# Kernel optimization log

Measured on AMD Instinct MI355X. Metric: run time of the kernel, lower is better.

The kernel has to match this reference:

```python
import jax, jax.numpy as jnp
import numpy as np

N = 50000
E = 800000
F_IN = 128
F_HID = 256   # 2 * out_channels
F_OUT = 128


def setup_inputs() -> dict:
    key = jax.random.key(0)
    ks = jax.random.split(key, 6)
    x = jax.random.normal(ks[0], (N, F_IN), dtype=jnp.float32)
    edge_index = jax.random.randint(ks[1], (2, E), 0, N, dtype=jnp.int64)
    # GCNConv params: glorot weight + zero bias (PyG default)
    s1 = (6.0 / (F_IN + F_HID)) ** 0.5
    s2 = (6.0 / (F_HID + F_OUT)) ** 0.5
    W1 = jax.random.uniform(ks[2], (F_IN, F_HID), jnp.float32, -s1, s1)
    b1 = jnp.zeros((F_HID,), jnp.float32)
    W2 = jax.random.uniform(ks[3], (F_HID, F_OUT), jnp.float32, -s2, s2)
    b2 = jnp.zeros((F_OUT,), jnp.float32)
    return {"x": x, "edge_index": edge_index, "W1": W1, "b1": b1, "W2": W2, "b2": b2}


def _gcn_conv(x, W, b, src, dst, deg_inv_sqrt, n):
    # norm per edge (self-loops already appended to src/dst)
    norm = deg_inv_sqrt[src] * deg_inv_sqrt[dst]          # [E+N]
    h = x @ W                                             # [N, F_out]
    msg = h[src] * norm[:, None]                          # [E+N, F_out] gather
    out = jax.ops.segment_sum(msg, dst, num_segments=n)   # scatter-add
    return out + b


def reference(x, edge_index, W1, b1, W2, b2):
    n = x.shape[0]
    loops = jnp.arange(n, dtype=edge_index.dtype)
    src = jnp.concatenate([edge_index[0], loops])
    dst = jnp.concatenate([edge_index[1], loops])
    # symmetric normalization with self-loops (PyG GCNConv default)
    deg = jax.ops.segment_sum(jnp.ones_like(dst, dtype=x.dtype), dst, num_segments=n)
    deg_inv_sqrt = jnp.where(deg > 0, jax.lax.rsqrt(jnp.maximum(deg, 1e-12)), 0.0)
    h = jax.nn.relu(_gcn_conv(x, W1, b1, src, dst, deg_inv_sqrt, n))
    h = jax.nn.relu(_gcn_conv(h, W2, b2, src, dst, deg_inv_sqrt, n))
    return h
```

## Files before the change

kernel.cpp:

```cpp
#include <hip/hip_runtime.h>


typedef short bf16x8 __attribute__((ext_vector_type(8)));
typedef float f32x4 __attribute__((ext_vector_type(4)));

#define LDSTRIDE 264
#define BSHIFT 7
#define BMASK 127

__device__ inline unsigned short f2bf(float f) {
    unsigned int u = __float_as_uint(f);
    u += 0x7FFF + ((u >> 16) & 1);
    return (unsigned short)(u >> 16);
}
__device__ inline float bf2f(unsigned short h) {
    return __uint_as_float(((unsigned int)h) << 16);
}

__device__ inline void swz1(const float* W, unsigned short* Ws, int K, int N, int i) {
    int k = i / N, n = i % N;
    int KC = K >> 5;
    size_t d = ((((size_t)(n >> 4) * KC + (k >> 5)) * 64) + ((k >> 3) & 3) * 16 + (n & 15)) * 8
               + (k & 7);
    Ws[d] = f2bf(W[i]);
}
__global__ void wswz_kernel(const float* __restrict__ W1, const float* __restrict__ W2,
                            unsigned short* __restrict__ W1s, unsigned short* __restrict__ W2s,
                            int* __restrict__ ctrl) {
    int i = blockIdx.x * blockDim.x + threadIdx.x;
    if (blockIdx.x == 0) {
        for (int j = threadIdx.x; j < 512; j += 256) ctrl[j] = 0;
    }
    if (i < 32768) swz1(W1, W1s, 128, 256, i);
    else if (i < 65536) swz1(W2, W2s, 256, 128, i - 32768);
}

__global__ __launch_bounds__(256) void bin_kernel(
    const int* __restrict__ src, const int* __restrict__ dst,
    int* __restrict__ bcur, unsigned int* __restrict__ bbuf,
    int E, int cap, int nbuck) {
    __shared__ int cnt[512];
    __shared__ int base[512];
    int t = threadIdx.x;
    for (int i = t; i < nbuck; i += 256) cnt[i] = 0;
    __syncthreads();
    int e0 = blockIdx.x * 2048;
    unsigned int p_[8];
    int b_[8];
#pragma unroll
    for (int i = 0; i < 8; i++) {
        int e = e0 + i * 256 + t;
        if (e < E) {
            int s = src[e], d = dst[e];
            b_[i] = d >> BSHIFT;
            p_[i] = ((unsigned)(d & BMASK) << 24) | (unsigned)s;
            atomicAdd(&cnt[b_[i]], 1);
        } else b_[i] = -1;
    }
    __syncthreads();
    for (int b = t; b < nbuck; b += 256) {
        int c = cnt[b];
        base[b] = (c > 0) ? atomicAdd(&bcur[b], c) : 0;
    }
    __syncthreads();
    for (int i = t; i < nbuck; i += 256) cnt[i] = 0;
    __syncthreads();
#pragma unroll
    for (int i = 0; i < 8; i++) {
        if (b_[i] >= 0) {
            int b = b_[i];
            int p = base[b] + atomicAdd(&cnt[b], 1);
            if (p >= 0 && p < cap) bbuf[(size_t)b * cap + p] = p_[i];
        }
    }
}

__global__ __launch_bounds__(256) void bucket_csr_kernel(
    const int* __restrict__ bcur, const unsigned int* __restrict__ bbuf,
    const float* __restrict__ x,
    int* __restrict__ col, int* __restrict__ rowbeg, int* __restrict__ rowend,
    float* __restrict__ dinv, unsigned short* __restrict__ Xs, int N, int cap) {
    __shared__ int ldeg[128];
    __shared__ int lrp[256];
    __shared__ float sdv[128];
    int b = blockIdx.x, t = threadIdx.x;
    int cnt = min(max(bcur[b], 0), cap);
    if (t < 128) ldeg[t] = 0;
    __syncthreads();
    const unsigned int* mybuf = bbuf + (size_t)b * cap;
    for (int i = t; i < cnt; i += 256)
        atomicAdd(&ldeg[mybuf[i] >> 24], 1);
    __syncthreads();
    int v = (t < 128) ? ldeg[t] : 0;
    lrp[t] = v;
    __syncthreads();
    for (int off = 1; off < 128; off <<= 1) {
        int u = (t >= off) ? lrp[t - off] : 0;
        __syncthreads();
        lrp[t] += u;
        __syncthreads();
    }
    int excl = lrp[t] - v;
    int gbase = b * cap;
    if (t < 128) {
        int r = b * 128 + t;
        float dv = rsqrtf((float)v + 1.0f);
        sdv[t] = dv;
        if (r < N) {
            rowbeg[r] = gbase + excl;
            rowend[r] = gbase + excl + v;
            dinv[r] = dv;
        }
        ldeg[t] = excl;
    }
    __syncthreads();
    for (int i = t; i < cnt; i += 256) {
        unsigned int pr = mybuf[i];
        int p = atomicAdd(&ldeg[pr >> 24], 1);
        col[gbase + p] = (int)(pr & 0xffffffu);
    }
    int rbase = b * 128;
    for (int i = t; i < 128 * 32; i += 256) {
        int rl = i >> 5;
        int gr = rbase + rl;
        if (gr >= N) break;
        float s = sdv[rl];
        float4 xv = ((const float4*)x)[(size_t)gr * 32 + (i & 31)];
        ushort4 o;
        o.x = f2bf(xv.x * s); o.y = f2bf(xv.y * s);
        o.z = f2bf(xv.z * s); o.w = f2bf(xv.w * s);
        ((ushort4*)Xs)[(size_t)gr * 32 + (i & 31)] = o;
    }
}

__global__ __launch_bounds__(256) void gather2_kernel(
    const int* __restrict__ rowbeg, const int* __restrict__ rowend,
    const int* __restrict__ col, const unsigned short* __restrict__ P,
    const float* __restrict__ dinv, const float* __restrict__ bias,
    float* __restrict__ OF, int N) {
    int gid = blockIdx.x * blockDim.x + threadIdx.x;
    int r = gid >> 5;
    if (r >= N) return;
    int lane = gid & 31;
    const size_t off = (size_t)lane * 4;
    const unsigned short* Pf = P + off;

    ushort4 u = *(const ushort4*)(Pf + (size_t)r * 128);
    float ax = bf2f(u.x), ay = bf2f(u.y), az = bf2f(u.z), aw = bf2f(u.w);

    int beg = rowbeg[r], end = rowend[r];
    int i = beg;
    for (; i + 7 < end; i += 8) {
        ushort4 v0 = *(const ushort4*)(Pf + (size_t)col[i + 0] * 128);
        ushort4 v1 = *(const ushort4*)(Pf + (size_t)col[i + 1] * 128);
        ushort4 v2 = *(const ushort4*)(Pf + (size_t)col[i + 2] * 128);
        ushort4 v3 = *(const ushort4*)(Pf + (size_t)col[i + 3] * 128);
        ushort4 v4 = *(const ushort4*)(Pf + (size_t)col[i + 4] * 128);
        ushort4 v5 = *(const ushort4*)(Pf + (size_t)col[i + 5] * 128);
        ushort4 v6 = *(const ushort4*)(Pf + (size_t)col[i + 6] * 128);
        ushort4 v7 = *(const ushort4*)(Pf + (size_t)col[i + 7] * 128);
        ax += bf2f(v0.x) + bf2f(v1.x) + bf2f(v2.x) + bf2f(v3.x)
            + bf2f(v4.x) + bf2f(v5.x) + bf2f(v6.x) + bf2f(v7.x);
        ay += bf2f(v0.y) + bf2f(v1.y) + bf2f(v2.y) + bf2f(v3.y)
            + bf2f(v4.y) + bf2f(v5.y) + bf2f(v6.y) + bf2f(v7.y);
        az += bf2f(v0.z) + bf2f(v1.z) + bf2f(v2.z) + bf2f(v3.z)
            + bf2f(v4.z) + bf2f(v5.z) + bf2f(v6.z) + bf2f(v7.z);
        aw += bf2f(v0.w) + bf2f(v1.w) + bf2f(v2.w) + bf2f(v3.w)
            + bf2f(v4.w) + bf2f(v5.w) + bf2f(v6.w) + bf2f(v7.w);
    }
    for (; i < end; i++) {
        ushort4 a = *(const ushort4*)(Pf + (size_t)col[i] * 128);
        ax += bf2f(a.x); ay += bf2f(a.y); az += bf2f(a.z); aw += bf2f(a.w);
    }
    float s = dinv[r];
    float4 bb = *(const float4*)(bias + off);
    float4 o;
    o.x = fmaxf(ax * s + bb.x, 0.f);
    o.y = fmaxf(ay * s + bb.y, 0.f);
    o.z = fmaxf(az * s + bb.z, 0.f);
    o.w = fmaxf(aw * s + bb.w, 0.f);
    *(float4*)(OF + (size_t)r * 128 + off) = o;
}

__global__ __launch_bounds__(256, 4) void gemm_fused_kernel(
    const int* __restrict__ rowbeg, const int* __restrict__ rowend,
    const int* __restrict__ col, const unsigned short* __restrict__ Xs,
    const unsigned short* __restrict__ W1s, const unsigned short* __restrict__ W2s,
    const float* __restrict__ bias, const float* __restrict__ dinv,
    unsigned short* __restrict__ T, int M) {
    __shared__ unsigned short lh[4][16 * LDSTRIDE];
    int wave = threadIdx.x >> 6;
    int lane = threadIdx.x & 63;
    int mt = blockIdx.x * 4 + wave;
    int m0 = mt * 16;
    bool active = (m0 < M);
    int mrow = lane & 15, quad = lane >> 4;
    unsigned short* myl = lh[wave];

    if (active) {
        int rr = m0 + mrow; if (rr >= M) rr = M - 1;
        float acc[4][8];
        const unsigned short* base = Xs + quad * 8;
#pragma unroll
        for (int kc = 0; kc < 4; kc++) {
            bf16x8 v = *(const bf16x8*)(base + (size_t)rr * 128 + kc * 32);
#pragma unroll
            for (int j = 0; j < 8; j++) acc[kc][j] = bf2f((unsigned short)v[j]);
        }
        int beg = rowbeg[rr], end = rowend[rr];
        int i = beg;
        for (; i + 3 < end; i += 4) {
            size_t c0 = (size_t)col[i] * 128, c1 = (size_t)col[i + 1] * 128;
            size_t c2 = (size_t)col[i + 2] * 128, c3 = (size_t)col[i + 3] * 128;
            bf16x8 p0 = *(const bf16x8*)(base + c0);
            bf16x8 p1 = *(const bf16x8*)(base + c0 + 32);
            bf16x8 p2 = *(const bf16x8*)(base + c0 + 64);
            bf16x8 p3 = *(const bf16x8*)(base + c0 + 96);
            bf16x8 q0 = *(const bf16x8*)(base + c1);
            bf16x8 q1 = *(const bf16x8*)(base + c1 + 32);
            bf16x8 q2 = *(const bf16x8*)(base + c1 + 64);
            bf16x8 q3 = *(const bf16x8*)(base + c1 + 96);
            bf16x8 r0 = *(const bf16x8*)(base + c2);
            bf16x8 r1 = *(const bf16x8*)(base + c2 + 32);
            bf16x8 r2 = *(const bf16x8*)(base + c2 + 64);
            bf16x8 r3 = *(const bf16x8*)(base + c2 + 96);
            bf16x8 s0 = *(const bf16x8*)(base + c3);
            bf16x8 s1 = *(const bf16x8*)(base + c3 + 32);
            bf16x8 s2 = *(const bf16x8*)(base + c3 + 64);
            bf16x8 s3 = *(const bf16x8*)(base + c3 + 96);
#pragma unroll
            for (int j = 0; j < 8; j++) {
                acc[0][j] += (bf2f((unsigned short)p0[j]) + bf2f((unsigned short)q0[j]))
                           + (bf2f((unsigned short)r0[j]) + bf2f((unsigned short)s0[j]));
                acc[1][j] += (bf2f((unsigned short)p1[j]) + bf2f((unsigned short)q1[j]))
                           + (bf2f((unsigned short)r1[j]) + bf2f((unsigned short)s1[j]));
                acc[2][j] += (bf2f((unsigned short)p2[j]) + bf2f((unsigned short)q2[j]))
                           + (bf2f((unsigned short)r2[j]) + bf2f((unsigned short)s2[j]));
                acc[3][j] += (bf2f((unsigned short)p3[j]) + bf2f((unsigned short)q3[j]))
                           + (bf2f((unsigned short)r3[j]) + bf2f((unsigned short)s3[j]));
            }
        }
        for (; i + 1 < end; i += 2) {
            size_t c0 = (size_t)col[i] * 128, c1 = (size_t)col[i + 1] * 128;
            bf16x8 p0 = *(const bf16x8*)(base + c0);
            bf16x8 p1 = *(const bf16x8*)(base + c0 + 32);
            bf16x8 p2 = *(const bf16x8*)(base + c0 + 64);
            bf16x8 p3 = *(const bf16x8*)(base + c0 + 96);
            bf16x8 q0 = *(const bf16x8*)(base + c1);
            bf16x8 q1 = *(const bf16x8*)(base + c1 + 32);
            bf16x8 q2 = *(const bf16x8*)(base + c1 + 64);
            bf16x8 q3 = *(const bf16x8*)(base + c1 + 96);
#pragma unroll
            for (int j = 0; j < 8; j++) {
                acc[0][j] += bf2f((unsigned short)p0[j]) + bf2f((unsigned short)q0[j]);
                acc[1][j] += bf2f((unsigned short)p1[j]) + bf2f((unsigned short)q1[j]);
                acc[2][j] += bf2f((unsigned short)p2[j]) + bf2f((unsigned short)q2[j]);
                acc[3][j] += bf2f((unsigned short)p3[j]) + bf2f((unsigned short)q3[j]);
            }
        }
        if (i < end) {
            size_t c0 = (size_t)col[i] * 128;
#pragma unroll
            for (int kc = 0; kc < 4; kc++) {
                bf16x8 p = *(const bf16x8*)(base + c0 + kc * 32);
#pragma unroll
                for (int j = 0; j < 8; j++) acc[kc][j] += bf2f((unsigned short)p[j]);
            }
        }
        float dvr = dinv[rr];
        bf16x8 a[4];
#pragma unroll
        for (int kc = 0; kc < 4; kc++)
#pragma unroll
            for (int j = 0; j < 8; j++)
                a[kc][j] = (short)f2bf(acc[kc][j] * dvr);

        float dv[4];
#pragma unroll
        for (int i2 = 0; i2 < 4; i2++) {
            int gr = m0 + quad * 4 + i2;
            dv[i2] = dinv[gr < M ? gr : M - 1];
        }
        const bf16x8* w1v = (const bf16x8*)W1s;
        for (int nt = 0; nt < 16; nt++) {
            f32x4 c = {0.f, 0.f, 0.f, 0.f};
#pragma unroll
            for (int kc = 0; kc < 4; kc++) {
                bf16x8 b = w1v[(nt * 4 + kc) * 64 + lane];
                c = __builtin_amdgcn_mfma_f32_16x16x32_bf16(a[kc], b, c, 0, 0, 0);
            }
            int colc = nt * 16 + mrow;
            float bb = bias[colc];
#pragma unroll
            for (int i2 = 0; i2 < 4; i2++) {
                float v = fmaxf(c[i2] + bb, 0.f) * dv[i2];
                myl[(quad * 4 + i2) * LDSTRIDE + colc] = f2bf(v);
            }
        }
    }
    __syncthreads();
    if (active) {
        bf16x8 h[8];
        const unsigned short* hrow = myl + mrow * LDSTRIDE + quad * 8;
#pragma unroll
        for (int kc = 0; kc < 8; kc++) h[kc] = *(const bf16x8*)(hrow + kc * 32);
        const bf16x8* w2v = (const bf16x8*)W2s;
        for (int nt = 0; nt < 8; nt++) {
            f32x4 c = {0.f, 0.f, 0.f, 0.f};
#pragma unroll
            for (int kc = 0; kc < 8; kc++) {
                bf16x8 b = w2v[(nt * 8 + kc) * 64 + lane];
                c = __builtin_amdgcn_mfma_f32_16x16x32_bf16(h[kc], b, c, 0, 0, 0);
            }
            int colc = nt * 16 + mrow;
#pragma unroll
            for (int i2 = 0; i2 < 4; i2++) {
                int gr = m0 + quad * 4 + i2;
                if (gr < M) T[(size_t)gr * 128 + colc] = f2bf(c[i2]);
            }
        }
    }
}

extern "C" void kernel_launch(void* const* d_in, const int* in_sizes, int n_in,
                              void* d_out, int out_size, void* d_ws, size_t ws_size,
                              hipStream_t stream) {
    const float* x  = (const float*)d_in[0];
    const int* ei   = (const int*)d_in[1];
    const float* W1 = (const float*)d_in[2];
    const float* b1 = (const float*)d_in[3];
    const float* W2 = (const float*)d_in[4];
    const float* b2 = (const float*)d_in[5];
    float* out      = (float*)d_out;

    const int N = in_sizes[0] / 128;
    const int E = in_sizes[1] / 2;
    const int* src = ei;
    const int* dst = ei + E;

    const int nbuck = (N + BMASK) >> BSHIFT;
    const int cap = E / nbuck + E / (4 * nbuck) + 512;

    float* ws = (float*)d_ws;
    size_t Np = ((size_t)N + 255) & ~(size_t)255;
    float*          dinv = ws;
    unsigned short* Ts   = (unsigned short*)(dinv + Np);
    unsigned short* Xs   = Ts + (size_t)N * 128;
    unsigned short* W1s  = Xs + (size_t)N * 128;
    unsigned short* W2s  = W1s + 32768;
    int* rowbeg = (int*)(W2s + 32768);
    int* rowend = rowbeg + Np;
    int* ctrl   = rowend + Np;
    int* bcur   = ctrl;
    unsigned int* bbuf = (unsigned int*)(ctrl + 512);
    int* col    = (int*)(bbuf + (size_t)nbuck * cap);

    wswz_kernel<<<256, 256, 0, stream>>>(W1, W2, W1s, W2s, ctrl);
    int nbins = (E + 2047) / 2048;
    bin_kernel<<<nbins, 256, 0, stream>>>(src, dst, bcur, bbuf, E, cap, nbuck);
    bucket_csr_kernel<<<nbuck, 256, 0, stream>>>(bcur, bbuf, x, col, rowbeg, rowend,
                                                 dinv, Xs, N, cap);

    int mtiles = (N + 15) / 16;
    gemm_fused_kernel<<<(mtiles + 3) / 4, 256, 0, stream>>>(rowbeg, rowend, col, Xs,
                                                            W1s, W2s, b1, dinv, Ts, N);

    int gth = N * 32;
    gather2_kernel<<<(gth + 255) / 256, 256, 0, stream>>>(rowbeg, rowend, col, Ts,
                                                          dinv, b2, out, N);
}
```

Baseline: 209.7 us.

## Split each 16-row tile across two waves for gather and both GEMMs

The fused aggregate+GEMM kernel now assigns one 16-row tile to a 128-thread block of two waves instead of four independent tiles per 256-thread block. Each wave gathers half of every row's neighbor list, and the partial sums are combined through LDS. The two waves then split the output columns of both MFMA GEMMs. The intent is to double parallelism per tile and shorten the latency-bound gather chain, at the cost of extra LDS traffic, three block barriers and more launched blocks.

```diff
diff --git a/kernel.cpp b/kernel.cpp
--- a/kernel.cpp
+++ b/kernel.cpp
@@ -182,142 +182,176 @@
     *(float4*)(OF + (size_t)r * 128 + off) = o;
 }
 
-__global__ __launch_bounds__(256, 4) void gemm_fused_kernel(
+__global__ __launch_bounds__(128, 6) void gemm_fused_kernel(
     const int* __restrict__ rowbeg, const int* __restrict__ rowend,
     const int* __restrict__ col, const unsigned short* __restrict__ Xs,
     const unsigned short* __restrict__ W1s, const unsigned short* __restrict__ W2s,
     const float* __restrict__ bias, const float* __restrict__ dinv,
     unsigned short* __restrict__ T, int M) {
-    __shared__ unsigned short lh[4][16 * LDSTRIDE];
+    __shared__ unsigned short afr[16 * 136];
+    __shared__ float part[16 * 132];
+    unsigned short* Hl = (unsigned short*)part;
+
     int wave = threadIdx.x >> 6;
     int lane = threadIdx.x & 63;
-    int mt = blockIdx.x * 4 + wave;
-    int m0 = mt * 16;
-    bool active = (m0 < M);
+    int m0 = blockIdx.x * 16;
     int mrow = lane & 15, quad = lane >> 4;
-    unsigned short* myl = lh[wave];
-
-    if (active) {
-        int rr = m0 + mrow; if (rr >= M) rr = M - 1;
-        float acc[4][8];
-        const unsigned short* base = Xs + quad * 8;
+
+    int rr = m0 + mrow; if (rr >= M) rr = M - 1;
+    float acc[4][8];
+    const unsigned short* base = Xs + quad * 8;
+    int beg = rowbeg[rr], end = rowend[rr];
+    int half = (end - beg) >> 1;
+    int b0 = wave ? (beg + half) : beg;
+    int e0 = wave ? end : (beg + half);
+
+    if (wave == 0) {
 #pragma unroll
         for (int kc = 0; kc < 4; kc++) {
             bf16x8 v = *(const bf16x8*)(base + (size_t)rr * 128 + kc * 32);
 #pragma unroll
             for (int j = 0; j < 8; j++) acc[kc][j] = bf2f((unsigned short)v[j]);
         }
-        int beg = rowbeg[rr], end = rowend[rr];
-        int i = beg;
-        for (; i + 3 < end; i += 4) {
-            size_t c0 = (size_t)col[i] * 128, c1 = (size_t)col[i + 1] * 128;
-            size_t c2 = (size_t)col[i + 2] * 128, c3 = (size_t)col[i + 3] * 128;
-            bf16x8 p0 = *(const bf16x8*)(base + c0);
-            bf16x8 p1 = *(const bf16x8*)(base + c0 + 32);
-            bf16x8 p2 = *(const bf16x8*)(base + c0 + 64);
-            bf16x8 p3 = *(const bf16x8*)(base + c0 + 96);
-            bf16x8 q0 = *(const bf16x8*)(base + c1);
-            bf16x8 q1 = *(const bf16x8*)(base + c1 + 32);
-            bf16x8 q2 = *(const bf16x8*)(base + c1 + 64);
-            bf16x8 q3 = *(const bf16x8*)(base + c1 + 96);
-            bf16x8 r0 = *(const bf16x8*)(base + c2);
-            bf16x8 r1 = *(const bf16x8*)(base + c2 + 32);
-            bf16x8 r2 = *(const bf16x8*)(base + c2 + 64);
-            bf16x8 r3 = *(const bf16x8*)(base + c2 + 96);
-            bf16x8 s0 = *(const bf16x8*)(base + c3);
-            bf16x8 s1 = *(const bf16x8*)(base + c3 + 32);
-            bf16x8 s2 = *(const bf16x8*)(base + c3 + 64);
-            bf16x8 s3 = *(const bf16x8*)(base + c3 + 96);
-#pragma unroll
-            for (int j = 0; j < 8; j++) {
-                acc[0][j] += (bf2f((unsigned short)p0[j]) + bf2f((unsigned short)q0[j]))
-                           + (bf2f((unsigned short)r0[j]) + bf2f((unsigned short)s0[j]));
-                acc[1][j] += (bf2f((unsigned short)p1[j]) + bf2f((unsigned short)q1[j]))
-                           + (bf2f((unsigned short)r1[j]) + bf2f((unsigned short)s1[j]));
-                acc[2][j] += (bf2f((unsigned short)p2[j]) + bf2f((unsigned short)q2[j]))
-                           + (bf2f((unsigned short)r2[j]) + bf2f((unsigned short)s2[j]));
-                acc[3][j] += (bf2f((unsigned short)p3[j]) + bf2f((unsigned short)q3[j]))
-                           + (bf2f((unsigned short)r3[j]) + bf2f((unsigned short)s3[j]));
+    } else {
+#pragma unroll
+        for (int kc = 0; kc < 4; kc++)
+#pragma unroll
+            for (int j = 0; j < 8; j++) acc[kc][j] = 0.f;
+    }
+
+    int i = b0;
+    for (; i + 3 < e0; i += 4) {
+        size_t c0 = (size_t)col[i] * 128, c1 = (size_t)col[i + 1] * 128;
+        size_t c2 = (size_t)col[i + 2] * 128, c3 = (size_t)col[i + 3] * 128;
+        bf16x8 p0 = *(const bf16x8*)(base + c0);
+        bf16x8 p1 = *(const bf16x8*)(base + c0 + 32);
+        bf16x8 p2 = *(const bf16x8*)(base + c0 + 64);
+        bf16x8 p3 = *(const bf16x8*)(base + c0 + 96);
+        bf16x8 q0 = *(const bf16x8*)(base + c1);
+        bf16x8 q1 = *(const bf16x8*)(base + c1 + 32);
+        bf16x8 q2 = *(const bf16x8*)(base + c1 + 64);
+        bf16x8 q3 = *(const bf16x8*)(base + c1 + 96);
+        bf16x8 r0 = *(const bf16x8*)(base + c2);
+        bf16x8 r1 = *(const bf16x8*)(base + c2 + 32);
+        bf16x8 r2 = *(const bf16x8*)(base + c2 + 64);
+        bf16x8 r3 = *(const bf16x8*)(base + c2 + 96);
+        bf16x8 s0 = *(const bf16x8*)(base + c3);
+        bf16x8 s1 = *(const bf16x8*)(base + c3 + 32);
+        bf16x8 s2 = *(const bf16x8*)(base + c3 + 64);
+        bf16x8 s3 = *(const bf16x8*)(base + c3 + 96);
+#pragma unroll
+        for (int j = 0; j < 8; j++) {
+            acc[0][j] += (bf2f((unsigned short)p0[j]) + bf2f((unsigned short)q0[j]))
+                       + (bf2f((unsigned short)r0[j]) + bf2f((unsigned short)s0[j]));
+            acc[1][j] += (bf2f((unsigned short)p1[j]) + bf2f((unsigned short)q1[j]))
+                       + (bf2f((unsigned short)r1[j]) + bf2f((unsigned short)s1[j]));
+            acc[2][j] += (bf2f((unsigned short)p2[j]) + bf2f((unsigned short)q2[j]))
+                       + (bf2f((unsigned short)r2[j]) + bf2f((unsigned short)s2[j]));
+            acc[3][j] += (bf2f((unsigned short)p3[j]) + bf2f((unsigned short)q3[j]))
+                       + (bf2f((unsigned short)r3[j]) + bf2f((unsigned short)s3[j]));
+        }
+    }
+    for (; i + 1 < e0; i += 2) {
+        size_t c0 = (size_t)col[i] * 128, c1 = (size_t)col[i + 1] * 128;
+        bf16x8 p0 = *(const bf16x8*)(base + c0);
+        bf16x8 p1 = *(const bf16x8*)(base + c0 + 32);
+        bf16x8 p2 = *(const bf16x8*)(base + c0 + 64);
+        bf16x8 p3 = *(const bf16x8*)(base + c0 + 96);
+        bf16x8 q0 = *(const bf16x8*)(base + c1);
+        bf16x8 q1 = *(const bf16x8*)(base + c1 + 32);
+        bf16x8 q2 = *(const bf16x8*)(base + c1 + 64);
+        bf16x8 q3 = *(const bf16x8*)(base + c1 + 96);
+#pragma unroll
+        for (int j = 0; j < 8; j++) {
+            acc[0][j] += bf2f((unsigned short)p0[j]) + bf2f((unsigned short)q0[j]);
+            acc[1][j] += bf2f((unsigned short)p1[j]) + bf2f((unsigned short)q1[j]);
+            acc[2][j] += bf2f((unsigned short)p2[j]) + bf2f((unsigned short)q2[j]);
+            acc[3][j] += bf2f((unsigned short)p3[j]) + bf2f((unsigned short)q3[j]);
+        }
+    }
+    if (i < e0) {
+        size_t c0 = (size_t)col[i] * 128;
+#pragma unroll
+        for (int kc = 0; kc < 4; kc++) {
+            bf16x8 p = *(const bf16x8*)(base + c0 + kc * 32);
+#pragma unroll
+            for (int j = 0; j < 8; j++) acc[kc][j] += bf2f((unsigned short)p[j]);
+        }
+    }
+
+    if (wave == 1) {
+#pragma unroll
+        for (int kc = 0; kc < 4; kc++) {
+            f32x4 lo = {acc[kc][0], acc[kc][1], acc[kc][2], acc[kc][3]};
+            f32x4 hi = {acc[kc][4], acc[kc][5], acc[kc][6], acc[kc][7]};
+            *(f32x4*)(part + mrow * 132 + kc * 32 + quad * 8) = lo;
+            *(f32x4*)(part + mrow * 132 + kc * 32 + quad * 8 + 4) = hi;
+        }
+    }
+    __syncthreads();
+    bf16x8 a[4];
+    if (wave == 0) {
+        float dvr = dinv[rr];
+#pragma unroll
+        for (int kc = 0; kc < 4; kc++) {
+            f32x4 lo = *(const f32x4*)(part + mrow * 132 + kc * 32 + quad * 8);
+            f32x4 hi = *(const f32x4*)(part + mrow * 132 + kc * 32 + quad * 8 + 4);
+#pragma unroll
+            for (int j = 0; j < 4; j++) {
+                a[kc][j]     = (short)f2bf((acc[kc][j]     + lo[j]) * dvr);
+                a[kc][j + 4] = (short)f2bf((acc[kc][j + 4] + hi[j]) * dvr);
             }
-        }
-        for (; i + 1 < end; i += 2) {
-            size_t c0 = (size_t)col[i] * 128, c1 = (size_t)col[i + 1] * 128;
-            bf16x8 p0 = *(const bf16x8*)(base + c0);
-            bf16x8 p1 = *(const bf16x8*)(base + c0 + 32);
-            bf16x8 p2 = *(const bf16x8*)(base + c0 + 64);
-            bf16x8 p3 = *(const bf16x8*)(base + c0 + 96);
-            bf16x8 q0 = *(const bf16x8*)(base + c1);
-            bf16x8 q1 = *(const bf16x8*)(base + c1 + 32);
-            bf16x8 q2 = *(const bf16x8*)(base + c1 + 64);
-            bf16x8 q3 = *(const bf16x8*)(base + c1 + 96);
-#pragma unroll
-            for (int j = 0; j < 8; j++) {
-                acc[0][j] += bf2f((unsigned short)p0[j]) + bf2f((unsigned short)q0[j]);
-                acc[1][j] += bf2f((unsigned short)p1[j]) + bf2f((unsigned short)q1[j]);
-                acc[2][j] += bf2f((unsigned short)p2[j]) + bf2f((unsigned short)q2[j]);
-                acc[3][j] += bf2f((unsigned short)p3[j]) + bf2f((unsigned short)q3[j]);
-            }
-        }
-        if (i < end) {
-            size_t c0 = (size_t)col[i] * 128;
-#pragma unroll
-            for (int kc = 0; kc < 4; kc++) {
-                bf16x8 p = *(const bf16x8*)(base + c0 + kc * 32);
-#pragma unroll
-                for (int j = 0; j < 8; j++) acc[kc][j] += bf2f((unsigned short)p[j]);
-            }
-        }
-        float dvr = dinv[rr];
-        bf16x8 a[4];
+            *(bf16x8*)(afr + mrow * 136 + kc * 32 + quad * 8) = a[kc];
+        }
+    }
+    __syncthreads();
+    if (wave == 1) {
 #pragma unroll
         for (int kc = 0; kc < 4; kc++)
-#pragma unroll
-            for (int j = 0; j < 8; j++)
-                a[kc][j] = (short)f2bf(acc[kc][j] * dvr);
-
-        float dv[4];
+            a[kc] = *(const bf16x8*)(afr + mrow * 136 + kc * 32 + quad * 8);
+    }
+
+    float dv[4];
+#pragma unroll
+    for (int i2 = 0; i2 < 4; i2++) {
+        int gr = m0 + quad * 4 + i2;
+        dv[i2] = dinv[gr < M ? gr : M - 1];
+    }
+    const bf16x8* w1v = (const bf16x8*)W1s;
+    for (int nt = wave * 8; nt < wave * 8 + 8; nt++) {
+        f32x4 c = {0.f, 0.f, 0.f, 0.f};
+#pragma unroll
+        for (int kc = 0; kc < 4; kc++) {
+            bf16x8 b = w1v[(nt * 4 + kc) * 64 + lane];
+            c = __builtin_amdgcn_mfma_f32_16x16x32_bf16(a[kc], b, c, 0, 0, 0);
+        }
+        int colc = nt * 16 + mrow;
+        float bb = bias[colc];
+#pragma unroll
+        for (int i2 = 0; i2 < 4; i2++) {
+            float v = fmaxf(c[i2] + bb, 0.f) * dv[i2];
+            Hl[(quad * 4 + i2) * LDSTRIDE + colc] = f2bf(v);
+        }
+    }
+    __syncthreads();
+
+    bf16x8 hh[8];
+    const unsigned short* hrow = Hl + mrow * LDSTRIDE + quad * 8;
+#pragma unroll
+    for (int kc = 0; kc < 8; kc++) hh[kc] = *(const bf16x8*)(hrow + kc * 32);
+    const bf16x8* w2v = (const bf16x8*)W2s;
+    for (int nt = wave * 4; nt < wave * 4 + 4; nt++) {
+        f32x4 c = {0.f, 0.f, 0.f, 0.f};
+#pragma unroll
+        for (int kc = 0; kc < 8; kc++) {
+            bf16x8 b = w2v[(nt * 8 + kc) * 64 + lane];
+            c = __builtin_amdgcn_mfma_f32_16x16x32_bf16(hh[kc], b, c, 0, 0, 0);
+        }
+        int colc = nt * 16 + mrow;
 #pragma unroll
         for (int i2 = 0; i2 < 4; i2++) {
             int gr = m0 + quad * 4 + i2;
-            dv[i2] = dinv[gr < M ? gr : M - 1];
-        }
-        const bf16x8* w1v = (const bf16x8*)W1s;
-        for (int nt = 0; nt < 16; nt++) {
-            f32x4 c = {0.f, 0.f, 0.f, 0.f};
-#pragma unroll
-            for (int kc = 0; kc < 4; kc++) {
-                bf16x8 b = w1v[(nt * 4 + kc) * 64 + lane];
-                c = __builtin_amdgcn_mfma_f32_16x16x32_bf16(a[kc], b, c, 0, 0, 0);
-            }
-            int colc = nt * 16 + mrow;
-            float bb = bias[colc];
-#pragma unroll
-            for (int i2 = 0; i2 < 4; i2++) {
-                float v = fmaxf(c[i2] + bb, 0.f) * dv[i2];
-                myl[(quad * 4 + i2) * LDSTRIDE + colc] = f2bf(v);
-            }
-        }
-    }
-    __syncthreads();
-    if (active) {
-        bf16x8 h[8];
-        const unsigned short* hrow = myl + mrow * LDSTRIDE + quad * 8;
-#pragma unroll
-        for (int kc = 0; kc < 8; kc++) h[kc] = *(const bf16x8*)(hrow + kc * 32);
-        const bf16x8* w2v = (const bf16x8*)W2s;
-        for (int nt = 0; nt < 8; nt++) {
-            f32x4 c = {0.f, 0.f, 0.f, 0.f};
-#pragma unroll
-            for (int kc = 0; kc < 8; kc++) {
-                bf16x8 b = w2v[(nt * 8 + kc) * 64 + lane];
-                c = __builtin_amdgcn_mfma_f32_16x16x32_bf16(h[kc], b, c, 0, 0, 0);
-            }
-            int colc = nt * 16 + mrow;
-#pragma unroll
-            for (int i2 = 0; i2 < 4; i2++) {
-                int gr = m0 + quad * 4 + i2;
-                if (gr < M) T[(size_t)gr * 128 + colc] = f2bf(c[i2]);
-            }
+            if (gr < M) T[(size_t)gr * 128 + colc] = f2bf(c[i2]);
         }
     }
 }
@@ -362,8 +396,8 @@
                                                  dinv, Xs, N, cap);
 
     int mtiles = (N + 15) / 16;
-    gemm_fused_kernel<<<(mtiles + 3) / 4, 256, 0, stream>>>(rowbeg, rowend, col, Xs,
-                                                            W1s, W2s, b1, dinv, Ts, N);
+    gemm_fused_kernel<<<mtiles, 128, 0, stream>>>(rowbeg, rowend, col, Xs,
+                                                  W1s, W2s, b1, dinv, Ts, N);
 
     int gth = N * 32;
     gather2_kernel<<<(gth + 255) / 256, 256, 0, stream>>>(rowbeg, rowend, col, Ts,
```

Result: slower. 332.4 us (+58.5%).

## Restructure fused GEMM: one 16-row tile per block, half-wave row gathers, split N across waves

Applied to the files above, without the earlier changes.

Each block now handles a single 16-row tile instead of four independent per-wave tiles. The neighbour aggregation assigns one row per half-wave, with each of 32 lanes loading 4 features, unrolled by 8 edges. The aggregated rows are staged in shared memory, and the MFMA output columns of both GEMMs are split across the four waves. The aim is to make the gather loads more coalesced per row and to spread the matmul work more evenly. The cost is extra syncthreads and LDS traffic, and the W fragments are now reloaded by four times as many blocks.

```diff
diff --git a/kernel.cpp b/kernel.cpp
--- a/kernel.cpp
+++ b/kernel.cpp
@@ -5,6 +5,7 @@
 typedef float f32x4 __attribute__((ext_vector_type(4)));
 
 #define LDSTRIDE 264
+#define XTSTRIDE 136
 #define BSHIFT 7
 #define BMASK 127
 
@@ -188,136 +189,105 @@
     const unsigned short* __restrict__ W1s, const unsigned short* __restrict__ W2s,
     const float* __restrict__ bias, const float* __restrict__ dinv,
     unsigned short* __restrict__ T, int M) {
-    __shared__ unsigned short lh[4][16 * LDSTRIDE];
-    int wave = threadIdx.x >> 6;
-    int lane = threadIdx.x & 63;
-    int mt = blockIdx.x * 4 + wave;
-    int m0 = mt * 16;
-    bool active = (m0 < M);
+    __shared__ unsigned short Xt[16 * XTSTRIDE];
+    __shared__ unsigned short Ht[16 * LDSTRIDE];
+
+    int t = threadIdx.x;
+    int m0 = blockIdx.x * 16;
+    int hw = t >> 5;
+    int l  = t & 31;
+    const unsigned short* Pf = Xs + (size_t)l * 4;
+
+#pragma unroll
+    for (int sub = 0; sub < 2; sub++) {
+        int lr = hw * 2 + sub;
+        int r = m0 + lr;
+        int rc = (r < M) ? r : (M - 1);
+        ushort4 u = *(const ushort4*)(Pf + (size_t)rc * 128);
+        float ax = bf2f(u.x), ay = bf2f(u.y), az = bf2f(u.z), aw = bf2f(u.w);
+        int beg = rowbeg[rc], end = rowend[rc];
+        int i = beg;
+        for (; i + 7 < end; i += 8) {
+            ushort4 v0 = *(const ushort4*)(Pf + (size_t)col[i + 0] * 128);
+            ushort4 v1 = *(const ushort4*)(Pf + (size_t)col[i + 1] * 128);
+            ushort4 v2 = *(const ushort4*)(Pf + (size_t)col[i + 2] * 128);
+            ushort4 v3 = *(const ushort4*)(Pf + (size_t)col[i + 3] * 128);
+            ushort4 v4 = *(const ushort4*)(Pf + (size_t)col[i + 4] * 128);
+            ushort4 v5 = *(const ushort4*)(Pf + (size_t)col[i + 5] * 128);
+            ushort4 v6 = *(const ushort4*)(Pf + (size_t)col[i + 6] * 128);
+            ushort4 v7 = *(const ushort4*)(Pf + (size_t)col[i + 7] * 128);
+            ax += bf2f(v0.x) + bf2f(v1.x) + bf2f(v2.x) + bf2f(v3.x)
+                + bf2f(v4.x) + bf2f(v5.x) + bf2f(v6.x) + bf2f(v7.x);
+            ay += bf2f(v0.y) + bf2f(v1.y) + bf2f(v2.y) + bf2f(v3.y)
+                + bf2f(v4.y) + bf2f(v5.y) + bf2f(v6.y) + bf2f(v7.y);
+            az += bf2f(v0.z) + bf2f(v1.z) + bf2f(v2.z) + bf2f(v3.z)
+                + bf2f(v4.z) + bf2f(v5.z) + bf2f(v6.z) + bf2f(v7.z);
+            aw += bf2f(v0.w) + bf2f(v1.w) + bf2f(v2.w) + bf2f(v3.w)
+                + bf2f(v4.w) + bf2f(v5.w) + bf2f(v6.w) + bf2f(v7.w);
+        }
+        for (; i < end; i++) {
+            ushort4 a = *(const ushort4*)(Pf + (size_t)col[i] * 128);
+            ax += bf2f(a.x); ay += bf2f(a.y); az += bf2f(a.z); aw += bf2f(a.w);
+        }
+        float dvr = dinv[rc];
+        ushort4 o;
+        o.x = f2bf(ax * dvr); o.y = f2bf(ay * dvr);
+        o.z = f2bf(az * dvr); o.w = f2bf(aw * dvr);
+        *(ushort4*)(Xt + lr * XTSTRIDE + l * 4) = o;
+    }
+    __syncthreads();
+
+    int wave = t >> 6;
+    int lane = t & 63;
     int mrow = lane & 15, quad = lane >> 4;
-    unsigned short* myl = lh[wave];
-
-    if (active) {
-        int rr = m0 + mrow; if (rr >= M) rr = M - 1;
-        float acc[4][8];
-        const unsigned short* base = Xs + quad * 8;
+
+    bf16x8 a[4];
+#pragma unroll
+    for (int kc = 0; kc < 4; kc++)
+        a[kc] = *(const bf16x8*)(Xt + mrow * XTSTRIDE + kc * 32 + quad * 8);
+
+    float dv[4];
+#pragma unroll
+    for (int i2 = 0; i2 < 4; i2++) {
+        int gr = m0 + quad * 4 + i2;
+        dv[i2] = dinv[gr < M ? gr : M - 1];
+    }
+
+    const bf16x8* w1v = (const bf16x8*)W1s;
+    for (int nt = wave * 4; nt < wave * 4 + 4; nt++) {
+        f32x4 c = {0.f, 0.f, 0.f, 0.f};
 #pragma unroll
         for (int kc = 0; kc < 4; kc++) {
-            bf16x8 v = *(const bf16x8*)(base + (size_t)rr * 128 + kc * 32);
-#pragma unroll
-            for (int j = 0; j < 8; j++) acc[kc][j] = bf2f((unsigned short)v[j]);
-        }
-        int beg = rowbeg[rr], end = rowend[rr];
-        int i = beg;
-        for (; i + 3 < end; i += 4) {
-            size_t c0 = (size_t)col[i] * 128, c1 = (size_t)col[i + 1] * 128;
-            size_t c2 = (size_t)col[i + 2] * 128, c3 = (size_t)col[i + 3] * 128;
-            bf16x8 p0 = *(const bf16x8*)(base + c0);
-            bf16x8 p1 = *(const bf16x8*)(base + c0 + 32);
-            bf16x8 p2 = *(const bf16x8*)(base + c0 + 64);
-            bf16x8 p3 = *(const bf16x8*)(base + c0 + 96);
-            bf16x8 q0 = *(const bf16x8*)(base + c1);
-            bf16x8 q1 = *(const bf16x8*)(base + c1 + 32);
-            bf16x8 q2 = *(const bf16x8*)(base + c1 + 64);
-            bf16x8 q3 = *(const bf16x8*)(base + c1 + 96);
-            bf16x8 r0 = *(const bf16x8*)(base + c2);
-            bf16x8 r1 = *(const bf16x8*)(base + c2 + 32);
-            bf16x8 r2 = *(const bf16x8*)(base + c2 + 64);
-            bf16x8 r3 = *(const bf16x8*)(base + c2 + 96);
-            bf16x8 s0 = *(const bf16x8*)(base + c3);
-            bf16x8 s1 = *(const bf16x8*)(base + c3 + 32);
-            bf16x8 s2 = *(const bf16x8*)(base + c3 + 64);
-            bf16x8 s3 = *(const bf16x8*)(base + c3 + 96);
-#pragma unroll
-            for (int j = 0; j < 8; j++) {
-                acc[0][j] += (bf2f((unsigned short)p0[j]) + bf2f((unsigned short)q0[j]))
-                           + (bf2f((unsigned short)r0[j]) + bf2f((unsigned short)s0[j]));
-                acc[1][j] += (bf2f((unsigned short)p1[j]) + bf2f((unsigned short)q1[j]))
-                           + (bf2f((unsigned short)r1[j]) + bf2f((unsigned short)s1[j]));
-                acc[2][j] += (bf2f((unsigned short)p2[j]) + bf2f((unsigned short)q2[j]))
-                           + (bf2f((unsigned short)r2[j]) + bf2f((unsigned short)s2[j]));
-                acc[3][j] += (bf2f((unsigned short)p3[j]) + bf2f((unsigned short)q3[j]))
-                           + (bf2f((unsigned short)r3[j]) + bf2f((unsigned short)s3[j]));
-            }
-        }
-        for (; i + 1 < end; i += 2) {
-            size_t c0 = (size_t)col[i] * 128, c1 = (size_t)col[i + 1] * 128;
-            bf16x8 p0 = *(const bf16x8*)(base + c0);
-            bf16x8 p1 = *(const bf16x8*)(base + c0 + 32);
-            bf16x8 p2 = *(const bf16x8*)(base + c0 + 64);
-            bf16x8 p3 = *(const bf16x8*)(base + c0 + 96);
-            bf16x8 q0 = *(const bf16x8*)(base + c1);
-            bf16x8 q1 = *(const bf16x8*)(base + c1 + 32);
-            bf16x8 q2 = *(const bf16x8*)(base + c1 + 64);
-            bf16x8 q3 = *(const bf16x8*)(base + c1 + 96);
-#pragma unroll
-            for (int j = 0; j < 8; j++) {
-                acc[0][j] += bf2f((unsigned short)p0[j]) + bf2f((unsigned short)q0[j]);
-                acc[1][j] += bf2f((unsigned short)p1[j]) + bf2f((unsigned short)q1[j]);
-                acc[2][j] += bf2f((unsigned short)p2[j]) + bf2f((unsigned short)q2[j]);
-                acc[3][j] += bf2f((unsigned short)p3[j]) + bf2f((unsigned short)q3[j]);
-            }
-        }
-        if (i < end) {
-            size_t c0 = (size_t)col[i] * 128;
-#pragma unroll
-            for (int kc = 0; kc < 4; kc++) {
-                bf16x8 p = *(const bf16x8*)(base + c0 + kc * 32);
-#pragma unroll
-                for (int j = 0; j < 8; j++) acc[kc][j] += bf2f((unsigned short)p[j]);
-            }
-        }
-        float dvr = dinv[rr];
-        bf16x8 a[4];
-#pragma unroll
-        for (int kc = 0; kc < 4; kc++)
-#pragma unroll
-            for (int j = 0; j < 8; j++)
-                a[kc][j] = (short)f2bf(acc[kc][j] * dvr);
-
-        float dv[4];
+            bf16x8 b = w1v[(nt * 4 + kc) * 64 + lane];
+            c = __builtin_amdgcn_mfma_f32_16x16x32_bf16(a[kc], b, c, 0, 0, 0);
+        }
+        int colc = nt * 16 + mrow;
+        float bb = bias[colc];
+#pragma unroll
+        for (int i2 = 0; i2 < 4; i2++) {
+            float v = fmaxf(c[i2] + bb, 0.f) * dv[i2];
+            Ht[(quad * 4 + i2) * LDSTRIDE + colc] = f2bf(v);
+        }
+    }
+    __syncthreads();
+
+    bf16x8 hh[8];
+    const unsigned short* hrow = Ht + mrow * LDSTRIDE + quad * 8;
+#pragma unroll
+    for (int kc = 0; kc < 8; kc++) hh[kc] = *(const bf16x8*)(hrow + kc * 32);
+    const bf16x8* w2v = (const bf16x8*)W2s;
+    for (int nt = wave * 2; nt < wave * 2 + 2; nt++) {
+        f32x4 c = {0.f, 0.f, 0.f, 0.f};
+#pragma unroll
+        for (int kc = 0; kc < 8; kc++) {
+            bf16x8 b = w2v[(nt * 8 + kc) * 64 + lane];
+            c = __builtin_amdgcn_mfma_f32_16x16x32_bf16(hh[kc], b, c, 0, 0, 0);
+        }
+        int colc = nt * 16 + mrow;
 #pragma unroll
         for (int i2 = 0; i2 < 4; i2++) {
             int gr = m0 + quad * 4 + i2;
-            dv[i2] = dinv[gr < M ? gr : M - 1];
-        }
-        const bf16x8* w1v = (const bf16x8*)W1s;
-        for (int nt = 0; nt < 16; nt++) {
-            f32x4 c = {0.f, 0.f, 0.f, 0.f};
-#pragma unroll
-            for (int kc = 0; kc < 4; kc++) {
-                bf16x8 b = w1v[(nt * 4 + kc) * 64 + lane];
-                c = __builtin_amdgcn_mfma_f32_16x16x32_bf16(a[kc], b, c, 0, 0, 0);
-            }
-            int colc = nt * 16 + mrow;
-            float bb = bias[colc];
-#pragma unroll
-            for (int i2 = 0; i2 < 4; i2++) {
-                float v = fmaxf(c[i2] + bb, 0.f) * dv[i2];
-                myl[(quad * 4 + i2) * LDSTRIDE + colc] = f2bf(v);
-            }
-        }
-    }
-    __syncthreads();
-    if (active) {
-        bf16x8 h[8];
-        const unsigned short* hrow = myl + mrow * LDSTRIDE + quad * 8;
-#pragma unroll
-        for (int kc = 0; kc < 8; kc++) h[kc] = *(const bf16x8*)(hrow + kc * 32);
-        const bf16x8* w2v = (const bf16x8*)W2s;
-        for (int nt = 0; nt < 8; nt++) {
-            f32x4 c = {0.f, 0.f, 0.f, 0.f};
-#pragma unroll
-            for (int kc = 0; kc < 8; kc++) {
-                bf16x8 b = w2v[(nt * 8 + kc) * 64 + lane];
-                c = __builtin_amdgcn_mfma_f32_16x16x32_bf16(h[kc], b, c, 0, 0, 0);
-            }
-            int colc = nt * 16 + mrow;
-#pragma unroll
-            for (int i2 = 0; i2 < 4; i2++) {
-                int gr = m0 + quad * 4 + i2;
-                if (gr < M) T[(size_t)gr * 128 + colc] = f2bf(c[i2]);
-            }
+            if (gr < M) T[(size_t)gr * 128 + colc] = f2bf(c[i2]);
         }
     }
 }
@@ -362,8 +332,8 @@
                                                  dinv, Xs, N, cap);
 
     int mtiles = (N + 15) / 16;
-    gemm_fused_kernel<<<(mtiles + 3) / 4, 256, 0, stream>>>(rowbeg, rowend, col, Xs,
-                                                            W1s, W2s, b1, dinv, Ts, N);
+    gemm_fused_kernel<<<mtiles, 256, 0, stream>>>(rowbeg, rowend, col, Xs,
+                                                  W1s, W2s, b1, dinv, Ts, N);
 
     int gth = N * 32;
     gather2_kernel<<<(gth + 255) / 256, 256, 0, stream>>>(rowbeg, rowend, col, Ts,
```

Result: faster. 199.4 us (-4.9%).
